# Kernel optimization log

Hardware: AMD Instinct MI355X
Metric: run time of the kernel (lower is better)

The kernel has to match this reference:

```python
import jax, jax.numpy as jnp
import numpy as np

N = 50000      # nodes
E = 800000     # edges (avg degree 16)
D = 64         # num_hidden
H = 4          # heads
OUT = 64       # out_dim

def setup_inputs() -> dict:
    key = jax.random.key(0)
    k = jax.random.split(key, 5)
    h = jax.random.normal(k[0], (N, D), dtype=jnp.float32)
    edge_index = jax.random.randint(k[1], (2, E), 0, N)
    gate_w = jax.random.normal(k[2], (H, 2 * D), dtype=jnp.float32) * 0.1  # per-head gate Linear weight
    gate_b = jnp.zeros((H,), dtype=jnp.float32)
    W_cat = jax.random.normal(k[3], (OUT, H * D), dtype=jnp.float32) * 0.05
    b_cat = jnp.zeros((OUT,), dtype=jnp.float32)
    return dict(h=h, edge_index=edge_index, gate_w=gate_w, gate_b=gate_b, W_cat=W_cat, b_cat=b_cat)

def reference(h, edge_index, gate_w, gate_b, W_cat, b_cat):
    # eval mode: both dropouts are identity
    row, col = edge_index[0], edge_index[1]
    n, d = h.shape
    # symmetric-ish degree normalization based on out-degree of row (as in original)
    deg = jax.ops.segment_sum(jnp.ones((row.shape[0],), dtype=h.dtype), row, num_segments=n)
    nd = jnp.clip(deg, 1.0) ** -0.5                     # [N]
    hr = h[row]                                          # [E, D] gather (source)
    hc = h[col]                                          # [E, D] gather (target)
    # per-head gate: tanh(Linear(cat(hr, hc))) vectorized over heads
    w1 = gate_w[:, :d]                                   # [H, D]
    w2 = gate_w[:, d:]                                   # [H, D]
    g = jnp.tanh(hr @ w1.T + hc @ w2.T + gate_b)        # [E, H]
    norm = g * (nd[row] * nd[col])[:, None]              # [E, H]
    # message: norm * x_j where x_j = h[source] = hr; aggregate (add) at target = col
    msgs = norm[:, :, None] * hr[:, None, :]             # [E, H, D]
    agg = jax.ops.segment_sum(msgs, col, num_segments=n) # [N, H, D]
    res = agg.reshape(n, -1)                             # concat heads -> [N, H*D]
    return jax.nn.relu(res @ W_cat.T + b_cat)            # [N, OUT]
```

## Files before the change

kernel.cpp:

```cpp
#include <hip/hip_runtime.h>

#define DD 64
#define HH 4
#define OUTC 64
#define CAP 48
#define CHUNK 4096

typedef __attribute__((ext_vector_type(8))) short bf16x8;
typedef __attribute__((ext_vector_type(4))) float f32x4;

__device__ __forceinline__ float fast_tanh(float x) {
    x = fminf(fmaxf(x, -15.f), 15.f);
    float e = __expf(2.f * x);
    return 1.f - 2.f / (e + 1.f);
}

__device__ __forceinline__ unsigned short f2bf(float f) {
    unsigned int u = __float_as_uint(f);
    u = (u + 0x7FFFu + ((u >> 16) & 1u)) >> 16;
    return (unsigned short)u;
}

__global__ __launch_bounds__(256) void partition_kernel(const int* __restrict__ row,
                                                        const int* __restrict__ col,
                                                        unsigned* __restrict__ cbuck,
                                                        unsigned char* __restrict__ rbuck,
                                                        int* __restrict__ ccount,
                                                        int* __restrict__ rcount,
                                                        int E, int NBUK, int BCAP, int nchunks) {
    __shared__ int hist[256];
    __shared__ int scn[256];
    __shared__ int gbase[256];
    __shared__ unsigned stage[CHUNK];
    __shared__ int saddr[CHUNK];
    int tid = threadIdx.x;
    int phaseC = (blockIdx.x < nchunks) ? 1 : 0;
    int chunk = phaseC ? blockIdx.x : blockIdx.x - nchunks;
    int e0 = chunk * CHUNK;
    int n = E - e0;
    if (n > CHUNK) n = CHUNK;
    const int* key = phaseC ? col : row;

    hist[tid] = 0;
    __syncthreads();
    for (int i = tid; i < n; i += 256) atomicAdd(&hist[key[e0 + i] >> 8], 1);
    __syncthreads();
    int v = hist[tid];
    scn[tid] = v;
    __syncthreads();
    for (int d = 1; d < 256; d <<= 1) {
        int a = (tid >= d) ? scn[tid - d] : 0;
        __syncthreads();
        scn[tid] += a;
        __syncthreads();
    }
    int excl = scn[tid] - v;
    scn[tid] = excl;
    if (tid < NBUK && v > 0)
        gbase[tid] = tid * BCAP + atomicAdd(phaseC ? &ccount[tid] : &rcount[tid], v);
    else
        gbase[tid] = tid * BCAP;
    hist[tid] = 0;
    __syncthreads();

    if (phaseC) {
        for (int i = tid; i < n; i += 256) {
            int c = col[e0 + i];
            int r = row[e0 + i];
            int b = c >> 8;
            int k = atomicAdd(&hist[b], 1);
            int p = scn[b] + k;
            stage[p] = ((unsigned)r << 8) | (unsigned)(c & 255);
            saddr[p] = gbase[b] + k;
        }
        __syncthreads();
        for (int i = tid; i < n; i += 256) cbuck[saddr[i]] = stage[i];
    } else {
        unsigned char* stB = (unsigned char*)stage;
        for (int i = tid; i < n; i += 256) {
            int r = row[e0 + i];
            int b = r >> 8;
            int k = atomicAdd(&hist[b], 1);
            int p = scn[b] + k;
            stB[p] = (unsigned char)(r & 255);
            saddr[p] = gbase[b] + k;
        }
        __syncthreads();
        for (int i = tid; i < n; i += 256) rbuck[saddr[i]] = stB[i];
    }
}

#define HSTR 68
__global__ __launch_bounds__(256) void local_prep(const unsigned* __restrict__ cbuck,
                                                  const unsigned char* __restrict__ rbuck,
                                                  const int* __restrict__ ccount,
                                                  const int* __restrict__ rcount,
                                                  int* __restrict__ cnt,
                                                  unsigned short* __restrict__ slots,
                                                  float* __restrict__ nd,
                                                  const float* __restrict__ h,
                                                  const float* __restrict__ gate_w,
                                                  const float* __restrict__ gate_b,
                                                  float* __restrict__ a12,
                                                  unsigned short* __restrict__ hbs,
                                                  int N, int NBUK, int BCAP) {
    __shared__ int cur[256];
    __shared__ float hs[256 * HSTR];
    __shared__ float gws[8 * 64];
    __shared__ float ndf[256];
    int tid = threadIdx.x;
    int b = blockIdx.x;
    cur[tid] = 0;
    __syncthreads();
    if (b < NBUK) {
        int s = ccount[b];
        if (s > BCAP) s = BCAP;
        const unsigned* src = cbuck + (size_t)b * BCAP;
        int node0 = b << 8;
        for (int i = tid; i < s; i += 256) {
            unsigned rc = src[i];
            int cl = rc & 255;
            int r = (int)(rc >> 8);
            int k = atomicAdd(&cur[cl], 1);
            if (k < CAP) slots[(size_t)(node0 + cl) * CAP + k] = (unsigned short)r;
        }
        __syncthreads();
        int node = node0 + tid;
        if (node < N) cnt[node] = cur[tid];
    } else {
        int bb = b - NBUK;
        int node0 = bb << 8;
        int nn = N - node0;
        if (nn > 256) nn = 256;
        int s = rcount[bb];
        if (s > BCAP) s = BCAP;
        const unsigned char* src = rbuck + (size_t)bb * BCAP;
        for (int i = tid; i < s; i += 256) atomicAdd(&cur[src[i]], 1);
        for (int i = tid; i < 512; i += 256) gws[i] = gate_w[i];
        int tile4 = nn * 16;
        const float4* hsrc = (const float4*)(h + (size_t)node0 * DD);
        for (int i = tid; i < tile4; i += 256) {
            int j = i >> 4, q = i & 15;
            *(float4*)&hs[j * HSTR + q * 4] = hsrc[i];
        }
        __syncthreads();
        int node = node0 + tid;
        if (tid < nn) {
            int dg = cur[tid];
            float ndv = rsqrtf((float)(dg < 1 ? 1 : dg));
            nd[node] = ndv;
            ndf[tid] = ndv;
        }
        __syncthreads();
        if (tid < nn) {
            float acc[8];
#pragma unroll
            for (int m = 0; m < 8; ++m) acc[m] = 0.f;
            const float4* hrow = (const float4*)&hs[tid * HSTR];
#pragma unroll
            for (int q = 0; q < 16; ++q) {
                float4 hv = hrow[q];
#pragma unroll
                for (int m = 0; m < 8; ++m) {
                    float4 gv = *(const float4*)&gws[m * 64 + q * 4];
                    acc[m] += hv.x * gv.x + hv.y * gv.y + hv.z * gv.z + hv.w * gv.w;
                }
            }
#pragma unroll
            for (int m = 0; m < 8; ++m) {
                int hd = m >> 1, part = m & 1;
                float vv = acc[m] + (part == 0 ? gate_b[hd] : 0.f);
                a12[(size_t)node * 8 + part * 4 + hd] = vv;
            }
        }
        for (int i = tid; i < tile4; i += 256) {
            int j = i >> 4, q = i & 15;
            float sc = ndf[j];
            const float* p = &hs[j * HSTR + q * 4];
            ushort4 pv;
            pv.x = f2bf(sc * p[0]);
            pv.y = f2bf(sc * p[1]);
            pv.z = f2bf(sc * p[2]);
            pv.w = f2bf(sc * p[3]);
            *(ushort4*)&hbs[(size_t)(node0 + j) * DD + q * 4] = pv;
        }
    }
}

__global__ __launch_bounds__(256) void gather_kernel(const int* __restrict__ cnt,
                                                     const unsigned short* __restrict__ slots,
                                                     const float* __restrict__ nd,
                                                     const float* __restrict__ a12,
                                                     const unsigned short* __restrict__ hbs,
                                                     unsigned short* __restrict__ aggb, int N) {
    __shared__ char lds[4 * 6912];
    int tid = threadIdx.x;
    int wv = tid >> 6;
    int lane = tid & 63;
    int quad = lane >> 4;
    int mcol = lane & 15;
    char* Alds = lds + wv * 6912;
    unsigned short* Au = (unsigned short*)Alds;
    int* rlds = (int*)(Alds + 6144);

    int gwave = (blockIdx.x * blockDim.x + tid) >> 6;
    int nwaves = (gridDim.x * blockDim.x) >> 6;
    int ngroups = (N + 3) >> 2;

    for (int g = gwave; g < ngroups; g += nwaves) {
        int c0 = g << 2;
        int o0 = 0, o1, o2, o3, o4;
        {
            int l0 = (c0 + 0 < N) ? cnt[c0 + 0] : 0; if (l0 > CAP) l0 = CAP;
            int l1 = (c0 + 1 < N) ? cnt[c0 + 1] : 0; if (l1 > CAP) l1 = CAP;
            int l2 = (c0 + 2 < N) ? cnt[c0 + 2] : 0; if (l2 > CAP) l2 = CAP;
            int l3 = (c0 + 3 < N) ? cnt[c0 + 3] : 0; if (l3 > CAP) l3 = CAP;
            o1 = l0; o2 = o1 + l1; o3 = o2 + l2; o4 = o3 + l3;
        }
        int K = o4;
        int ksteps = (K + 31) >> 5;
        for (int z = lane; z < ksteps * 256; z += 64) ((unsigned*)Au)[z] = 0u;
        for (int z = lane; z < ksteps * 32; z += 64) rlds[z] = 0;
        for (int p = lane; p < K; p += 64) {
            int i = (p >= o1) + (p >= o2) + (p >= o3);
            int c = c0 + i;
            int off = p - (i == 0 ? 0 : (i == 1 ? o1 : (i == 2 ? o2 : o3)));
            int r = slots[(size_t)c * CAP + off];
            rlds[p] = r;
            float4 a1 = *(const float4*)&a12[(size_t)r * 8];
            float4 a2 = *(const float4*)&a12[(size_t)c * 8 + 4];
            float t0 = fast_tanh(a1.x + a2.x);
            float t1 = fast_tanh(a1.y + a2.y);
            float t2 = fast_tanh(a1.z + a2.z);
            float t3 = fast_tanh(a1.w + a2.w);
            int bidx = (p >> 5) * 512 + ((p >> 3) & 3) * 128 + (p & 7);
            int m0 = i * 4;
            Au[bidx + (m0 + 0) * 8] = f2bf(t0);
            Au[bidx + (m0 + 1) * 8] = f2bf(t1);
            Au[bidx + (m0 + 2) * 8] = f2bf(t2);
            Au[bidx + (m0 + 3) * 8] = f2bf(t3);
        }
        f32x4 acc0 = (f32x4){0.f, 0.f, 0.f, 0.f};
        f32x4 acc1 = (f32x4){0.f, 0.f, 0.f, 0.f};
        f32x4 acc2 = (f32x4){0.f, 0.f, 0.f, 0.f};
        f32x4 acc3 = (f32x4){0.f, 0.f, 0.f, 0.f};
        for (int ks = 0; ks < ksteps; ++ks) {
            bf16x8 af = *(const bf16x8*)(Alds + ks * 1024 + lane * 16);
            int rk[8];
#pragma unroll
            for (int j = 0; j < 8; ++j) rk[j] = rlds[ks * 32 + quad * 8 + j];
#pragma unroll
            for (int nt = 0; nt < 4; ++nt) {
                const unsigned short* hp = hbs + nt * 16 + mcol;
                bf16x8 bf;
#pragma unroll
                for (int j = 0; j < 8; ++j) bf[j] = (short)hp[(size_t)rk[j] << 6];
                if (nt == 0) acc0 = __builtin_amdgcn_mfma_f32_16x16x32_bf16(af, bf, acc0, 0, 0, 0);
                else if (nt == 1) acc1 = __builtin_amdgcn_mfma_f32_16x16x32_bf16(af, bf, acc1, 0, 0, 0);
                else if (nt == 2) acc2 = __builtin_amdgcn_mfma_f32_16x16x32_bf16(af, bf, acc2, 0, 0, 0);
                else acc3 = __builtin_amdgcn_mfma_f32_16x16x32_bf16(af, bf, acc3, 0, 0, 0);
            }
        }
        int node = c0 + quad;
        if (node < N) {
            float ndv = nd[node];
            unsigned short* dst = aggb + (size_t)node * 256 + mcol;
#pragma unroll
            for (int reg = 0; reg < 4; ++reg) {
                dst[reg * 64 + 0] = f2bf(acc0[reg] * ndv);
                dst[reg * 64 + 16] = f2bf(acc1[reg] * ndv);
                dst[reg * 64 + 32] = f2bf(acc2[reg] * ndv);
                dst[reg * 64 + 48] = f2bf(acc3[reg] * ndv);
            }
        }
    }
}

__global__ __launch_bounds__(256) void gemm_kernel(const unsigned short* __restrict__ aggb,
                                                   const float* __restrict__ Wcat,
                                                   const float* __restrict__ b_cat,
                                                   float* __restrict__ out, int N) {
    __shared__ unsigned short WT[2048 * 8];
    int tid = threadIdx.x;
#pragma unroll
    for (int it = 0; it < 8; ++it) {
        int id = tid + it * 256;
        int ln = id & 63;
        int ks = (id >> 6) & 7;
        int ct = id >> 9;
        int o = ct * 16 + (ln & 15);
        int kb = ks * 32 + ((ln >> 4) & 3) * 8;
        const float4* src = (const float4*)&Wcat[(size_t)o * 256 + kb];
        float4 w0 = src[0];
        float4 w1 = src[1];
        ushort4* dst = (ushort4*)&WT[(size_t)id * 8];
        dst[0] = make_ushort4(f2bf(w0.x), f2bf(w0.y), f2bf(w0.z), f2bf(w0.w));
        dst[1] = make_ushort4(f2bf(w1.x), f2bf(w1.y), f2bf(w1.z), f2bf(w1.w));
    }
    __syncthreads();

    int lane = tid & 63;
    int wv = tid >> 6;
    int m = lane & 15;
    int q = lane >> 4;
    float bb[4];
#pragma unroll
    for (int ct = 0; ct < 4; ++ct) bb[ct] = b_cat[ct * 16 + m];

    int ntiles = (N + 15) >> 4;
    int wgid = blockIdx.x * 4 + wv;
    int nwaves = gridDim.x * 4;
    for (int tile = wgid; tile < ntiles; tile += nwaves) {
        int n0 = tile << 4;
        int node = n0 + m;
        bf16x8 afrag[8];
        bool ok = (node < N);
        const unsigned short* arow = aggb + (size_t)node * 256 + q * 8;
#pragma unroll
        for (int ks = 0; ks < 8; ++ks) {
            if (ok)
                afrag[ks] = *(const bf16x8*)(arow + ks * 32);
            else
                afrag[ks] = (bf16x8)(short)0;
        }
        f32x4 acc[4];
#pragma unroll
        for (int ct = 0; ct < 4; ++ct) acc[ct] = (f32x4){0.f, 0.f, 0.f, 0.f};
#pragma unroll
        for (int ks = 0; ks < 8; ++ks) {
#pragma unroll
            for (int ct = 0; ct < 4; ++ct) {
                bf16x8 bfrag = *(const bf16x8*)&WT[(size_t)((ct * 8 + ks) * 64 + lane) * 8];
                acc[ct] = __builtin_amdgcn_mfma_f32_16x16x32_bf16(afrag[ks], bfrag, acc[ct], 0, 0, 0);
            }
        }
#pragma unroll
        for (int reg = 0; reg < 4; ++reg) {
            int n = n0 + q * 4 + reg;
            if (n < N) {
#pragma unroll
                for (int ct = 0; ct < 4; ++ct) {
                    float v = acc[ct][reg] + bb[ct];
                    out[(size_t)n * OUTC + ct * 16 + m] = v > 0.f ? v : 0.f;
                }
            }
        }
    }
}

extern "C" void kernel_launch(void* const* d_in, const int* in_sizes, int n_in,
                              void* d_out, int out_size, void* d_ws, size_t ws_size,
                              hipStream_t stream) {
    const float* h      = (const float*)d_in[0];
    const int*   edge   = (const int*)d_in[1];
    const float* gate_w = (const float*)d_in[2];
    const float* gate_b = (const float*)d_in[3];
    const float* Wcat   = (const float*)d_in[4];
    const float* b_cat  = (const float*)d_in[5];
    int N = in_sizes[0] / DD;
    int E = in_sizes[1] / 2;
    const int* row = edge;
    const int* colp = edge + E;
    float* out = (float*)d_out;

    int NBUK = (N + 255) >> 8;
    int BCAP = ((2 * E / NBUK) + 63) & ~63;

    char* ws = (char*)d_ws;
    size_t off = 0;
    size_t pad = ((size_t)NBUK * 4 + 255) & ~255ull;
    int*   ccount = (int*)(ws + off); off += pad;
    int*   rcount = (int*)(ws + off); off += pad;
    int*   cnt    = (int*)(ws + off); off += (size_t)N * 4;
    float* nd     = (float*)(ws + off); off += (size_t)N * 4;
    float* a12    = (float*)(ws + off); off += (size_t)N * 32;
    unsigned short* slots = (unsigned short*)(ws + off); off += ((size_t)N * CAP * 2 + 255) & ~255ull;
    unsigned short* hbs  = (unsigned short*)(ws + off); off += (size_t)N * DD * 2;
    unsigned short* aggb = (unsigned short*)(ws + off);
    unsigned*      cbuck = (unsigned*)aggb;
    unsigned char* rbuck = (unsigned char*)((char*)aggb + (size_t)NBUK * BCAP * 4);

    hipMemsetAsync(ccount, 0, pad + (size_t)NBUK * 4, stream);

    int nchunks = (E + CHUNK - 1) / CHUNK;
    partition_kernel<<<2 * nchunks, 256, 0, stream>>>(row, colp, cbuck, rbuck, ccount, rcount,
                                                      E, NBUK, BCAP, nchunks);
    local_prep<<<2 * NBUK, 256, 0, stream>>>(cbuck, rbuck, ccount, rcount, cnt, slots, nd,
                                             h, gate_w, gate_b, a12, hbs, N, NBUK, BCAP);
    gather_kernel<<<3125, 256, 0, stream>>>(cnt, slots, nd, a12, hbs, aggb, N);
    gemm_kernel<<<256, 256, 0, stream>>>(aggb, Wcat, b_cat, out, N);
}
```

Before: 146.0 us.

## Fuse gather aggregation and output GEMM into one kernel via LDS tile

Merges the gather/aggregate kernel with the projection GEMM. Each block aggregates a 16-node tile into shared memory in bf16, then each wave computes one 16-column slice of the output with MFMA and writes relu output directly. This removes the global round trip of the N×256 bf16 aggregate buffer and one kernel launch. In exchange every block converts the full W_cat into LDS, uses more shared memory per block (lower occupancy), and adds two block barriers per tile.

```diff
diff --git a/kernel.cpp b/kernel.cpp
--- a/kernel.cpp
+++ b/kernel.cpp
@@ -187,29 +187,50 @@
     }
 }
 
-__global__ __launch_bounds__(256) void gather_kernel(const int* __restrict__ cnt,
-                                                     const unsigned short* __restrict__ slots,
-                                                     const float* __restrict__ nd,
-                                                     const float* __restrict__ a12,
-                                                     const unsigned short* __restrict__ hbs,
-                                                     unsigned short* __restrict__ aggb, int N) {
-    __shared__ char lds[4 * 6912];
+__global__ __launch_bounds__(256) void gg_kernel(const int* __restrict__ cnt,
+                                                 const unsigned short* __restrict__ slots,
+                                                 const float* __restrict__ nd,
+                                                 const float* __restrict__ a12,
+                                                 const unsigned short* __restrict__ hbs,
+                                                 const float* __restrict__ Wcat,
+                                                 const float* __restrict__ b_cat,
+                                                 float* __restrict__ out, int N) {
+    __shared__ unsigned short WT[2048 * 8];
+    __shared__ char glds[4 * 6912];
+    __shared__ unsigned short A2[16 * 264];
     int tid = threadIdx.x;
     int wv = tid >> 6;
     int lane = tid & 63;
     int quad = lane >> 4;
     int mcol = lane & 15;
-    char* Alds = lds + wv * 6912;
+
+#pragma unroll
+    for (int it = 0; it < 8; ++it) {
+        int id = tid + it * 256;
+        int ln = id & 63;
+        int ks = (id >> 6) & 7;
+        int ct = id >> 9;
+        int o = ct * 16 + (ln & 15);
+        int kb = ks * 32 + ((ln >> 4) & 3) * 8;
+        const float4* src = (const float4*)&Wcat[(size_t)o * 256 + kb];
+        float4 w0 = src[0];
+        float4 w1 = src[1];
+        ushort4* dst = (ushort4*)&WT[(size_t)id * 8];
+        dst[0] = make_ushort4(f2bf(w0.x), f2bf(w0.y), f2bf(w0.z), f2bf(w0.w));
+        dst[1] = make_ushort4(f2bf(w1.x), f2bf(w1.y), f2bf(w1.z), f2bf(w1.w));
+    }
+    float bb = b_cat[wv * 16 + mcol];
+    __syncthreads();
+
+    char* Alds = glds + wv * 6912;
     unsigned short* Au = (unsigned short*)Alds;
     int* rlds = (int*)(Alds + 6144);
 
-    int gwave = (blockIdx.x * blockDim.x + tid) >> 6;
-    int nwaves = (gridDim.x * blockDim.x) >> 6;
-    int ngroups = (N + 3) >> 2;
-
-    for (int g = gwave; g < ngroups; g += nwaves) {
-        int c0 = g << 2;
-        int o0 = 0, o1, o2, o3, o4;
+    int ntiles = (N + 15) >> 4;
+    for (int t = blockIdx.x; t < ntiles; t += gridDim.x) {
+        int n0 = t << 4;
+        int c0 = n0 + wv * 4;
+        int o1, o2, o3, o4;
         {
             int l0 = (c0 + 0 < N) ? cnt[c0 + 0] : 0; if (l0 > CAP) l0 = CAP;
             int l1 = (c0 + 1 < N) ? cnt[c0 + 1] : 0; if (l1 > CAP) l1 = CAP;
@@ -261,10 +282,11 @@
                 else acc3 = __builtin_amdgcn_mfma_f32_16x16x32_bf16(af, bf, acc3, 0, 0, 0);
             }
         }
-        int node = c0 + quad;
-        if (node < N) {
-            float ndv = nd[node];
-            unsigned short* dst = aggb + (size_t)node * 256 + mcol;
+        {
+            int node = c0 + quad;
+            int nl = wv * 4 + quad;
+            float ndv = (node < N) ? nd[node] : 0.f;
+            unsigned short* dst = &A2[nl * 264 + mcol];
 #pragma unroll
             for (int reg = 0; reg < 4; ++reg) {
                 dst[reg * 64 + 0] = f2bf(acc0[reg] * ndv);
@@ -273,78 +295,25 @@
                 dst[reg * 64 + 48] = f2bf(acc3[reg] * ndv);
             }
         }
-    }
-}
-
-__global__ __launch_bounds__(256) void gemm_kernel(const unsigned short* __restrict__ aggb,
-                                                   const float* __restrict__ Wcat,
-                                                   const float* __restrict__ b_cat,
-                                                   float* __restrict__ out, int N) {
-    __shared__ unsigned short WT[2048 * 8];
-    int tid = threadIdx.x;
-#pragma unroll
-    for (int it = 0; it < 8; ++it) {
-        int id = tid + it * 256;
-        int ln = id & 63;
-        int ks = (id >> 6) & 7;
-        int ct = id >> 9;
-        int o = ct * 16 + (ln & 15);
-        int kb = ks * 32 + ((ln >> 4) & 3) * 8;
-        const float4* src = (const float4*)&Wcat[(size_t)o * 256 + kb];
-        float4 w0 = src[0];
-        float4 w1 = src[1];
-        ushort4* dst = (ushort4*)&WT[(size_t)id * 8];
-        dst[0] = make_ushort4(f2bf(w0.x), f2bf(w0.y), f2bf(w0.z), f2bf(w0.w));
-        dst[1] = make_ushort4(f2bf(w1.x), f2bf(w1.y), f2bf(w1.z), f2bf(w1.w));
-    }
-    __syncthreads();
-
-    int lane = tid & 63;
-    int wv = tid >> 6;
-    int m = lane & 15;
-    int q = lane >> 4;
-    float bb[4];
-#pragma unroll
-    for (int ct = 0; ct < 4; ++ct) bb[ct] = b_cat[ct * 16 + m];
-
-    int ntiles = (N + 15) >> 4;
-    int wgid = blockIdx.x * 4 + wv;
-    int nwaves = gridDim.x * 4;
-    for (int tile = wgid; tile < ntiles; tile += nwaves) {
-        int n0 = tile << 4;
-        int node = n0 + m;
-        bf16x8 afrag[8];
-        bool ok = (node < N);
-        const unsigned short* arow = aggb + (size_t)node * 256 + q * 8;
-#pragma unroll
-        for (int ks = 0; ks < 8; ++ks) {
-            if (ok)
-                afrag[ks] = *(const bf16x8*)(arow + ks * 32);
-            else
-                afrag[ks] = (bf16x8)(short)0;
-        }
-        f32x4 acc[4];
-#pragma unroll
-        for (int ct = 0; ct < 4; ++ct) acc[ct] = (f32x4){0.f, 0.f, 0.f, 0.f};
-#pragma unroll
-        for (int ks = 0; ks < 8; ++ks) {
-#pragma unroll
-            for (int ct = 0; ct < 4; ++ct) {
-                bf16x8 bfrag = *(const bf16x8*)&WT[(size_t)((ct * 8 + ks) * 64 + lane) * 8];
-                acc[ct] = __builtin_amdgcn_mfma_f32_16x16x32_bf16(afrag[ks], bfrag, acc[ct], 0, 0, 0);
-            }
-        }
-#pragma unroll
-        for (int reg = 0; reg < 4; ++reg) {
-            int n = n0 + q * 4 + reg;
-            if (n < N) {
-#pragma unroll
-                for (int ct = 0; ct < 4; ++ct) {
-                    float v = acc[ct][reg] + bb[ct];
-                    out[(size_t)n * OUTC + ct * 16 + m] = v > 0.f ? v : 0.f;
+        __syncthreads();
+        {
+            f32x4 c4 = (f32x4){0.f, 0.f, 0.f, 0.f};
+#pragma unroll
+            for (int ks = 0; ks < 8; ++ks) {
+                bf16x8 af = *(const bf16x8*)&A2[mcol * 264 + ks * 32 + quad * 8];
+                bf16x8 bf = *(const bf16x8*)&WT[(size_t)((wv * 8 + ks) * 64 + lane) * 8];
+                c4 = __builtin_amdgcn_mfma_f32_16x16x32_bf16(af, bf, c4, 0, 0, 0);
+            }
+#pragma unroll
+            for (int reg = 0; reg < 4; ++reg) {
+                int n = n0 + quad * 4 + reg;
+                if (n < N) {
+                    float v = c4[reg] + bb;
+                    out[(size_t)n * OUTC + wv * 16 + mcol] = v > 0.f ? v : 0.f;
                 }
             }
         }
+        __syncthreads();
     }
 }
 
@@ -376,9 +345,9 @@
     float* a12    = (float*)(ws + off); off += (size_t)N * 32;
     unsigned short* slots = (unsigned short*)(ws + off); off += ((size_t)N * CAP * 2 + 255) & ~255ull;
     unsigned short* hbs  = (unsigned short*)(ws + off); off += (size_t)N * DD * 2;
-    unsigned short* aggb = (unsigned short*)(ws + off);
-    unsigned*      cbuck = (unsigned*)aggb;
-    unsigned char* rbuck = (unsigned char*)((char*)aggb + (size_t)NBUK * BCAP * 4);
+    char* scratch = ws + off;
+    unsigned*      cbuck = (unsigned*)scratch;
+    unsigned char* rbuck = (unsigned char*)(scratch + (size_t)NBUK * BCAP * 4);
 
     hipMemsetAsync(ccount, 0, pad + (size_t)NBUK * 4, stream);
 
@@ -387,6 +356,7 @@
                                                       E, NBUK, BCAP, nchunks);
     local_prep<<<2 * NBUK, 256, 0, stream>>>(cbuck, rbuck, ccount, rcount, cnt, slots, nd,
                                              h, gate_w, gate_b, a12, hbs, N, NBUK, BCAP);
-    gather_kernel<<<3125, 256, 0, stream>>>(cnt, slots, nd, a12, hbs, aggb, N);
-    gemm_kernel<<<256, 256, 0, stream>>>(aggb, Wcat, b_cat, out, N);
-}
+    int ntiles = (N + 15) >> 4;
+    int grid = (ntiles + 1) / 2;
+    gg_kernel<<<grid, 256, 0, stream>>>(cnt, slots, nd, a12, hbs, Wcat, b_cat, out, N);
+}
```

After: 165.3 us. 13.2% more time.

## Stage slot lists in LDS, split row-prep blocks in half, shrink partition chunks

Applied to the files above, without the earlier changes.

The column-bucket path now builds each bucket's slot lists in shared memory and writes them to global memory as coalesced 16-byte stores, instead of scattering 2-byte writes. The row path is split into two blocks per bucket of 128 nodes each, with two threads per node for the gate dot products. This raises parallelism and lowers per-block LDS use. The partition chunk size is halved to launch more blocks. Each row half-block still recounts the whole bucket's degrees, which is redundant work, and the slots buffer is padded to whole buckets.

```diff
diff --git a/kernel.cpp b/kernel.cpp
--- a/kernel.cpp
+++ b/kernel.cpp
@@ -4,7 +4,7 @@
 #define HH 4
 #define OUTC 64
 #define CAP 48
-#define CHUNK 4096
+#define CHUNK 2048
 
 typedef __attribute__((ext_vector_type(8))) short bf16x8;
 typedef __attribute__((ext_vector_type(4))) float f32x4;
@@ -104,15 +104,14 @@
                                                   float* __restrict__ a12,
                                                   unsigned short* __restrict__ hbs,
                                                   int N, int NBUK, int BCAP) {
-    __shared__ int cur[256];
-    __shared__ float hs[256 * HSTR];
-    __shared__ float gws[8 * 64];
-    __shared__ float ndf[256];
+    __shared__ char smem[38400];
     int tid = threadIdx.x;
     int b = blockIdx.x;
+    int* cur = (int*)smem;
     cur[tid] = 0;
     __syncthreads();
     if (b < NBUK) {
+        unsigned short* slds = (unsigned short*)(smem + 1024);
         int s = ccount[b];
         if (s > BCAP) s = BCAP;
         const unsigned* src = cbuck + (size_t)b * BCAP;
@@ -120,69 +119,78 @@
         for (int i = tid; i < s; i += 256) {
             unsigned rc = src[i];
             int cl = rc & 255;
-            int r = (int)(rc >> 8);
             int k = atomicAdd(&cur[cl], 1);
-            if (k < CAP) slots[(size_t)(node0 + cl) * CAP + k] = (unsigned short)r;
+            if (k < CAP) slds[cl * CAP + k] = (unsigned short)(rc >> 8);
         }
         __syncthreads();
         int node = node0 + tid;
         if (node < N) cnt[node] = cur[tid];
+        uint4* gdst = (uint4*)(slots + (size_t)node0 * CAP);
+        const uint4* gsrc = (const uint4*)slds;
+        for (int i = tid; i < 1536; i += 256) gdst[i] = gsrc[i];
     } else {
-        int bb = b - NBUK;
-        int node0 = bb << 8;
-        int nn = N - node0;
-        if (nn > 256) nn = 256;
+        float* gws = (float*)(smem + 1024);
+        float* ndf = (float*)(smem + 3072);
+        float* hs = (float*)(smem + 3584);
+        int idx = b - NBUK;
+        int bb = idx >> 1;
+        int half = idx & 1;
+        int node0h = (bb << 8) + half * 128;
         int s = rcount[bb];
         if (s > BCAP) s = BCAP;
         const unsigned char* src = rbuck + (size_t)bb * BCAP;
         for (int i = tid; i < s; i += 256) atomicAdd(&cur[src[i]], 1);
         for (int i = tid; i < 512; i += 256) gws[i] = gate_w[i];
+        int nn = N - node0h;
+        if (nn > 128) nn = 128;
+        if (nn < 0) nn = 0;
         int tile4 = nn * 16;
-        const float4* hsrc = (const float4*)(h + (size_t)node0 * DD);
+        const float4* hsrc = (const float4*)(h + (size_t)node0h * DD);
         for (int i = tid; i < tile4; i += 256) {
             int j = i >> 4, q = i & 15;
             *(float4*)&hs[j * HSTR + q * 4] = hsrc[i];
         }
         __syncthreads();
-        int node = node0 + tid;
         if (tid < nn) {
-            int dg = cur[tid];
+            int dg = cur[half * 128 + tid];
             float ndv = rsqrtf((float)(dg < 1 ? 1 : dg));
-            nd[node] = ndv;
+            nd[node0h + tid] = ndv;
             ndf[tid] = ndv;
         }
         __syncthreads();
-        if (tid < nn) {
-            float acc[8];
-#pragma unroll
-            for (int m = 0; m < 8; ++m) acc[m] = 0.f;
-            const float4* hrow = (const float4*)&hs[tid * HSTR];
+        int j = tid >> 1, sel = tid & 1;
+        if (j < nn) {
+            float acc[4];
+            acc[0] = acc[1] = acc[2] = acc[3] = 0.f;
+            const float4* hrow = (const float4*)&hs[j * HSTR];
 #pragma unroll
             for (int q = 0; q < 16; ++q) {
                 float4 hv = hrow[q];
 #pragma unroll
-                for (int m = 0; m < 8; ++m) {
-                    float4 gv = *(const float4*)&gws[m * 64 + q * 4];
+                for (int m = 0; m < 4; ++m) {
+                    float4 gv = *(const float4*)&gws[(sel * 4 + m) * 64 + q * 4];
                     acc[m] += hv.x * gv.x + hv.y * gv.y + hv.z * gv.z + hv.w * gv.w;
                 }
             }
-#pragma unroll
-            for (int m = 0; m < 8; ++m) {
-                int hd = m >> 1, part = m & 1;
+            int node = node0h + j;
+#pragma unroll
+            for (int m = 0; m < 4; ++m) {
+                int mm = sel * 4 + m;
+                int hd = mm >> 1, part = mm & 1;
                 float vv = acc[m] + (part == 0 ? gate_b[hd] : 0.f);
                 a12[(size_t)node * 8 + part * 4 + hd] = vv;
             }
         }
         for (int i = tid; i < tile4; i += 256) {
-            int j = i >> 4, q = i & 15;
-            float sc = ndf[j];
-            const float* p = &hs[j * HSTR + q * 4];
+            int j2 = i >> 4, q = i & 15;
+            float sc = ndf[j2];
+            const float* p = &hs[j2 * HSTR + q * 4];
             ushort4 pv;
             pv.x = f2bf(sc * p[0]);
             pv.y = f2bf(sc * p[1]);
             pv.z = f2bf(sc * p[2]);
             pv.w = f2bf(sc * p[3]);
-            *(ushort4*)&hbs[(size_t)(node0 + j) * DD + q * 4] = pv;
+            *(ushort4*)&hbs[(size_t)(node0h + j2) * DD + q * 4] = pv;
         }
     }
 }
@@ -209,7 +217,7 @@
 
     for (int g = gwave; g < ngroups; g += nwaves) {
         int c0 = g << 2;
-        int o0 = 0, o1, o2, o3, o4;
+        int o1, o2, o3, o4;
         {
             int l0 = (c0 + 0 < N) ? cnt[c0 + 0] : 0; if (l0 > CAP) l0 = CAP;
             int l1 = (c0 + 1 < N) ? cnt[c0 + 1] : 0; if (l1 > CAP) l1 = CAP;
@@ -374,7 +382,8 @@
     int*   cnt    = (int*)(ws + off); off += (size_t)N * 4;
     float* nd     = (float*)(ws + off); off += (size_t)N * 4;
     float* a12    = (float*)(ws + off); off += (size_t)N * 32;
-    unsigned short* slots = (unsigned short*)(ws + off); off += ((size_t)N * CAP * 2 + 255) & ~255ull;
+    unsigned short* slots = (unsigned short*)(ws + off);
+    off += ((size_t)NBUK * 256 * CAP * 2 + 255) & ~255ull;
     unsigned short* hbs  = (unsigned short*)(ws + off); off += (size_t)N * DD * 2;
     unsigned short* aggb = (unsigned short*)(ws + off);
     unsigned*      cbuck = (unsigned*)aggb;
@@ -385,7 +394,7 @@
     int nchunks = (E + CHUNK - 1) / CHUNK;
     partition_kernel<<<2 * nchunks, 256, 0, stream>>>(row, colp, cbuck, rbuck, ccount, rcount,
                                                       E, NBUK, BCAP, nchunks);
-    local_prep<<<2 * NBUK, 256, 0, stream>>>(cbuck, rbuck, ccount, rcount, cnt, slots, nd,
+    local_prep<<<3 * NBUK, 256, 0, stream>>>(cbuck, rbuck, ccount, rcount, cnt, slots, nd,
                                              h, gate_w, gate_b, a12, hbs, N, NBUK, BCAP);
     gather_kernel<<<3125, 256, 0, stream>>>(cnt, slots, nd, a12, hbs, aggb, N);
     gemm_kernel<<<256, 256, 0, stream>>>(aggb, Wcat, b_cat, out, N);
```

After: 141.3 us. 3.3% less time.
